# Kernel optimization log

Hardware: AMD Instinct MI355X
Metric: run time of the kernel (lower is better)

## Reference

```python
import jax, jax.numpy as jnp
import numpy as np

CHEB_K = 3
EMBED_DIM = 16
N_NODES = 2048
DIM = 64


def setup_inputs() -> dict:
    key = jax.random.key(0)
    k1, k2, k3, k4 = jax.random.split(key, 4)
    B, N, T, D = 16, N_NODES, 12, DIM
    x = jax.random.normal(k1, (B, N, T, D), dtype=jnp.float32)
    node_embeddings = jax.random.normal(k2, (N, EMBED_DIM), dtype=jnp.float32)
    # xavier-uniform-ish init for pools
    wp_bound = float(np.sqrt(6.0 / (EMBED_DIM * CHEB_K * D + D)))
    weights_pool = jax.random.uniform(k3, (EMBED_DIM, CHEB_K, D, D), dtype=jnp.float32,
                                      minval=-wp_bound, maxval=wp_bound)
    bias_pool = jax.random.uniform(k4, (EMBED_DIM, D), dtype=jnp.float32)
    return {"x": x, "node_embeddings": node_embeddings,
            "weights_pool": weights_pool, "bias_pool": bias_pool}


def reference(x, node_embeddings, weights_pool, bias_pool):
    B, N, T, D = x.shape
    cheb_k = weights_pool.shape[1]
    # [B,N,T,D] -> [B*T, N, D]
    xr = jnp.transpose(x, (0, 2, 1, 3)).reshape(B * T, N, D)
    # adaptive adjacency: row-softmax of relu gram matrix  [N,N]
    supports = jax.nn.softmax(jax.nn.relu(node_embeddings @ node_embeddings.T), axis=1)
    # Chebyshev polynomial basis of the adaptive support
    support_set = [jnp.eye(N, dtype=supports.dtype), supports]
    for _ in range(2, cheb_k):
        support_set.append(2.0 * supports @ support_set[-1] - support_set[-2])
    supports_k = jnp.stack(support_set, axis=0)  # [K,N,N]
    # hypernetwork: per-node weights/bias from embeddings
    weights = jnp.einsum('nd,dkio->nkio', node_embeddings, weights_pool)  # [N,K,D,D]
    bias = node_embeddings @ bias_pool  # [N,D]
    # graph conv: gather K-hop aggregates, then per-node grouped GEMM
    x_g = jnp.einsum('knm,bmc->bnkc', supports_k, xr)  # [B*T,N,K,D]
    x_gconv = jnp.einsum('bnki,nkio->bno', x_g, weights) + bias  # [B*T,N,D]
    return jnp.transpose(x_gconv.reshape(B, T, N, D), (0, 2, 1, 3))
```

## Files before the change

### kernel.cpp

```cpp
#include <hip/hip_runtime.h>
#include <hip/hip_bf16.h>

#define N_NODES 2048
#define EMB 16
#define NT 12
#define BT 192
#define C_COLS 12288
#define TD 768
#define BSTRIDE (N_NODES * TD)
#define KDIM 2048

typedef unsigned short u16;
typedef unsigned int u32;
typedef __attribute__((ext_vector_type(8))) __bf16 bf16x8;
typedef __attribute__((ext_vector_type(8))) u16 u16x8;
typedef __attribute__((ext_vector_type(4))) float f32x4;

__device__ __forceinline__ u16 f2bfu(float f) {
    u32 u = __float_as_uint(f);
    return (u16)((u + 0x7FFFu + ((u >> 16) & 1u)) >> 16);
}
__device__ __forceinline__ float bfu2f(u16 h) {
    return __uint_as_float(((u32)h) << 16);
}

__device__ __forceinline__ void gl2lds16(const void* g, void* l) {
    __builtin_amdgcn_global_load_lds(
        (const __attribute__((address_space(1))) u32*)g,
        (__attribute__((address_space(3))) u32*)l, 16, 0, 0);
}

__device__ __forceinline__ int cswz(int col, int row) {
    return (col & ~63) | ((((col >> 3) ^ row) & 7) << 3) | (col & 7);
}

__global__ void supports_kernel(const float* __restrict__ E, u16* __restrict__ Sb)
{
    __shared__ float en[EMB];
    __shared__ float red[256];
    const int n = blockIdx.x;
    const int tid = threadIdx.x;
    if (tid < EMB) en[tid] = E[n * EMB + tid];
    __syncthreads();

    float v[8];
    float mx = 0.0f;
    #pragma unroll
    for (int j = 0; j < 8; ++j) {
        const int m = tid + j * 256;
        const float* em = E + m * EMB;
        float acc = 0.f;
        #pragma unroll
        for (int d = 0; d < EMB; ++d) acc += en[d] * em[d];
        acc = fmaxf(acc, 0.f);
        v[j] = acc;
        mx = fmaxf(mx, acc);
    }
    red[tid] = mx;
    __syncthreads();
    for (int s = 128; s > 0; s >>= 1) {
        if (tid < s) red[tid] = fmaxf(red[tid], red[tid + s]);
        __syncthreads();
    }
    mx = red[0];
    __syncthreads();

    float sum = 0.f;
    #pragma unroll
    for (int j = 0; j < 8; ++j) { v[j] = __expf(v[j] - mx); sum += v[j]; }
    red[tid] = sum;
    __syncthreads();
    for (int s = 128; s > 0; s >>= 1) {
        if (tid < s) red[tid] += red[tid + s];
        __syncthreads();
    }
    const float inv = 1.f / red[0];
    #pragma unroll
    for (int j = 0; j < 8; ++j)
        Sb[(size_t)n * KDIM + tid + j * 256] = f2bfu(v[j] * inv);
}

__global__ void supports2_kernel(const float* __restrict__ E, u16* __restrict__ Sb)
{
    __shared__ float en[EMB];
    __shared__ float red[256];
    const int n = blockIdx.x;
    const int tid = threadIdx.x;
    if (tid < EMB) en[tid] = E[n * EMB + tid];
    __syncthreads();

    float v[8];
    float mx = 0.0f;
    #pragma unroll
    for (int j = 0; j < 8; ++j) {
        const int m = tid + j * 256;
        const float* em = E + m * EMB;
        float acc = 0.f;
        #pragma unroll
        for (int d = 0; d < EMB; ++d) acc += en[d] * em[d];
        acc = fmaxf(acc, 0.f);
        v[j] = acc;
        mx = fmaxf(mx, acc);
    }
    red[tid] = mx;
    __syncthreads();
    for (int s = 128; s > 0; s >>= 1) {
        if (tid < s) red[tid] = fmaxf(red[tid], red[tid + s]);
        __syncthreads();
    }
    mx = red[0];
    __syncthreads();

    float sum = 0.f;
    #pragma unroll
    for (int j = 0; j < 8; ++j) { v[j] = __expf(v[j] - mx); sum += v[j]; }
    red[tid] = sum;
    __syncthreads();
    for (int s = 128; s > 0; s >>= 1) {
        if (tid < s) red[tid] += red[tid + s];
        __syncthreads();
    }
    const float inv = 1.f / red[0];
    #pragma unroll
    for (int j = 0; j < 8; ++j) {
        const int m = tid + j * 256;
        Sb[(size_t)n * KDIM + cswz(m, n)] = f2bfu(v[j] * inv);
    }
}

__global__ void strans_kernel(const u16* __restrict__ Sb, u16* __restrict__ SbT)
{
    __shared__ u16 T[64][65];
    const int tid = threadIdx.x;
    const int n0 = blockIdx.y * 64;
    const int j0 = blockIdx.x * 64;
    const int lc = tid & 63;
    const int rg = tid >> 6;
    #pragma unroll
    for (int j = 0; j < 16; ++j) {
        const int r = j * 4 + rg;
        const u16 vv = Sb[(size_t)(n0 + r) * KDIM + j0 + lc];
        const int jt = ((((lc >> 3) ^ (n0 + r)) & 7) << 3) | (lc & 7);
        T[jt][r] = vv;
    }
    __syncthreads();
    #pragma unroll
    for (int j = 0; j < 16; ++j) {
        const int jj = j * 4 + rg;
        const int cs = ((((lc >> 3) ^ (j0 + jj)) & 7) << 3) | (lc & 7);
        SbT[(size_t)(j0 + jj) * KDIM + n0 + cs] = T[jj][lc];
    }
}

__global__ void xcast_kernel(const float* __restrict__ x, u16* __restrict__ XbT, int c0g)
{
    __shared__ u16 tile[64][65];
    const int tid = threadIdx.x;
    const int cg = c0g + blockIdx.x * 64;
    const int b = cg / TD;
    const int r0 = cg - b * TD;
    const int m0 = blockIdx.y * 64;
    const float* xp = x + (size_t)b * BSTRIDE + (size_t)m0 * TD + r0;

    const int lc = tid & 63;
    const int rg = tid >> 6;
    #pragma unroll
    for (int j = 0; j < 16; ++j) {
        const int mr = j * 4 + rg;
        tile[lc][mr] = f2bfu(xp[(size_t)mr * TD + lc]);
    }
    __syncthreads();
    u16* op = XbT + (size_t)(blockIdx.x * 64) * KDIM + m0;
    #pragma unroll
    for (int j = 0; j < 16; ++j) {
        const int cr = j * 4 + rg;
        op[(size_t)cr * KDIM + lc] = tile[cr][lc];
    }
}

__global__ void xcast2_kernel(const float* __restrict__ x, u16* __restrict__ XbT)
{
    __shared__ u16 tile[64][65];
    const int tid = threadIdx.x;
    const int cg = blockIdx.x * 64;
    const int b = cg / TD;
    const int r0 = cg - b * TD;
    const int m0 = blockIdx.y * 64;
    const float* xp = x + (size_t)b * BSTRIDE + (size_t)m0 * TD + r0;

    const int lc = tid & 63;
    const int rg = tid >> 6;
    #pragma unroll
    for (int j = 0; j < 16; ++j) {
        const int mr = j * 4 + rg;
        tile[lc][mr] = f2bfu(xp[(size_t)mr * TD + lc]);
    }
    __syncthreads();
    u16* op = XbT + (size_t)cg * KDIM + m0;
    #pragma unroll
    for (int j = 0; j < 16; ++j) {
        const int cr = j * 4 + rg;
        const int ls = ((((lc >> 3) ^ cr) & 7) << 3) | (lc & 7);
        op[(size_t)cr * KDIM + ls] = tile[cr][lc];
    }
}

template <int MODE>
__launch_bounds__(512, 2)
__global__ void gemm256(const u16* __restrict__ A, const u16* __restrict__ B,
                        u16* __restrict__ O1, u16* __restrict__ O2)
{
    __shared__ char smem[131072];
    const int tid = threadIdx.x;
    const int lane = tid & 63;
    const int w = tid >> 6;
    const int wm = w >> 2, wn = w & 3;
    const int ln15 = lane & 15, quad = lane >> 4;

    const int m0 = blockIdx.y * 256;
    const int c0 = blockIdx.x * 256;

    const int srow = lane >> 3;
    const int sbyte = (lane & 7) * 16;
    const char* gA = (const char*)A + (size_t)(m0 + w * 32 + srow) * 4096 + sbyte;
    const char* gB = (const char*)B + (size_t)(c0 + w * 32 + srow) * 4096 + sbyte;
    char* lA = smem + w * 4096;
    char* lB = smem + 32768 + w * 4096;

    auto stage = [&](int t, int buf) {
        #pragma unroll
        for (int j = 0; j < 4; ++j) {
            gl2lds16(gA + (size_t)j * 32768 + (size_t)t * 128,
                     lA + buf * 65536 + j * 1024);
            gl2lds16(gB + (size_t)j * 32768 + (size_t)t * 128,
                     lB + buf * 65536 + j * 1024);
        }
    };

    f32x4 acc[8][4] = {};
    const int arow0 = wm * 128 + ln15;
    const int brow0 = wn * 64 + ln15;
    const int xorm = (ln15 & 7) << 4;

    auto phase = [&](const char* Ab, const char* Bb, int kh) {
        const int koff = (kh * 64 + quad * 16) ^ xorm;
        bf16x8 af[8], bg[4];
        #pragma unroll
        for (int mi = 0; mi < 8; ++mi)
            af[mi] = *(const bf16x8*)(Ab + (arow0 + mi * 16) * 128 + koff);
        #pragma unroll
        for (int ni = 0; ni < 4; ++ni)
            bg[ni] = *(const bf16x8*)(Bb + (brow0 + ni * 16) * 128 + koff);
        asm volatile("s_waitcnt lgkmcnt(0)" ::: "memory");
        __builtin_amdgcn_sched_barrier(0);
        __builtin_amdgcn_s_setprio(1);
        #pragma unroll
        for (int mi = 0; mi < 8; ++mi)
            #pragma unroll
            for (int ni = 0; ni < 4; ++ni)
                acc[mi][ni] = __builtin_amdgcn_mfma_f32_16x16x32_bf16(
                    af[mi], bg[ni], acc[mi][ni], 0, 0, 0);
        __builtin_amdgcn_s_setprio(0);
        __builtin_amdgcn_sched_barrier(0);
        __builtin_amdgcn_s_barrier();
    };

    const char* b0A = smem;
    const char* b0B = smem + 32768;
    const char* b1A = smem + 65536;
    const char* b1B = smem + 98304;

    const int NTI = KDIM / 64;
    stage(0, 0);
    stage(1, 1);

    #pragma unroll 1
    for (int it = 0; it < NTI / 2; ++it) {
        const int t0 = 2 * it;
        if (it > 0) stage(t0 + 1, 1);
        asm volatile("s_waitcnt vmcnt(8)" ::: "memory");
        __builtin_amdgcn_sched_barrier(0);
        __builtin_amdgcn_s_barrier();

        phase(b0A, b0B, 0);
        phase(b0A, b0B, 1);

        if (t0 + 2 < NTI) {
            stage(t0 + 2, 0);
            asm volatile("s_waitcnt vmcnt(8)" ::: "memory");
        } else {
            asm volatile("s_waitcnt vmcnt(0)" ::: "memory");
        }
        __builtin_amdgcn_sched_barrier(0);
        __builtin_amdgcn_s_barrier();

        phase(b1A, b1B, 0);
        phase(b1A, b1B, 1);
    }

    const int mbase = m0 + wm * 128 + quad * 4;
    const int cbase = c0 + wn * 64 + ln15;
    if (MODE == 0) {
        #pragma unroll
        for (int mi = 0; mi < 8; ++mi) {
            #pragma unroll
            for (int ni = 0; ni < 4; ++ni) {
                const f32x4 v = acc[mi][ni];
                const int cc = cbase + ni * 16;
                #pragma unroll
                for (int r = 0; r < 4; ++r) {
                    const int mm = mbase + mi * 16 + r;
                    const float t2 = 2.f * v[r] - ((mm == cc) ? 1.f : 0.f);
                    O1[(size_t)mm * KDIM + cswz(cc, mm)] = f2bfu(t2);
                }
            }
        }
    } else {
        u16* Ob = (m0 < 2048) ? O1 : O2;
        const int mb = (m0 < 2048) ? mbase : (mbase - 2048);
        #pragma unroll
        for (int mi = 0; mi < 8; ++mi) {
            #pragma unroll
            for (int ni = 0; ni < 4; ++ni) {
                const f32x4 v = acc[mi][ni];
                const int cc = cbase + ni * 16;
                u16* orow = Ob + (size_t)(mb + mi * 16) * C_COLS + cc;
                orow[0 * C_COLS] = f2bfu(v.x);
                orow[1 * C_COLS] = f2bfu(v.y);
                orow[2 * C_COLS] = f2bfu(v.z);
                orow[3 * C_COLS] = f2bfu(v.w);
            }
        }
    }
}

__launch_bounds__(256, 2)
__global__ void gemm128s(const u16* __restrict__ A, const u16* __restrict__ B,
                         u16* __restrict__ O1)
{
    __shared__ char smem[65536];
    const int tid = threadIdx.x;
    const int lane = tid & 63;
    const int w = tid >> 6;
    const int wm = w >> 1, wn = w & 1;
    const int ln15 = lane & 15, quad = lane >> 4;

    const int m0 = blockIdx.y * 128;
    const int c0 = blockIdx.x * 128;

    const int srow = lane >> 3;
    const int sbyte = (lane & 7) * 16;
    const char* gA = (const char*)A + (size_t)(m0 + w * 32 + srow) * 4096 + sbyte;
    const char* gB = (const char*)B + (size_t)(c0 + w * 32 + srow) * 4096 + sbyte;
    char* lA = smem + w * 4096;
    char* lB = smem + 16384 + w * 4096;

    auto stage = [&](int t, int buf) {
        #pragma unroll
        for (int j = 0; j < 4; ++j) {
            gl2lds16(gA + (size_t)j * 32768 + (size_t)t * 128,
                     lA + buf * 32768 + j * 1024);
            gl2lds16(gB + (size_t)j * 32768 + (size_t)t * 128,
                     lB + buf * 32768 + j * 1024);
        }
    };

    f32x4 acc[4][4] = {};
    const int arow0 = wm * 64 + ln15;
    const int brow0 = wn * 64 + ln15;
    const int xorm = (ln15 & 7) << 4;

    auto phase = [&](const char* Ab, const char* Bb, int kh) {
        const int koff = (kh * 64 + quad * 16) ^ xorm;
        bf16x8 af[4], bg[4];
        #pragma unroll
        for (int mi = 0; mi < 4; ++mi)
            af[mi] = *(const bf16x8*)(Ab + (arow0 + mi * 16) * 128 + koff);
        #pragma unroll
        for (int ni = 0; ni < 4; ++ni)
            bg[ni] = *(const bf16x8*)(Bb + (brow0 + ni * 16) * 128 + koff);
        asm volatile("s_waitcnt lgkmcnt(0)" ::: "memory");
        __builtin_amdgcn_sched_barrier(0);
        __builtin_amdgcn_s_setprio(1);
        #pragma unroll
        for (int mi = 0; mi < 4; ++mi)
            #pragma unroll
            for (int ni = 0; ni < 4; ++ni)
                acc[mi][ni] = __builtin_amdgcn_mfma_f32_16x16x32_bf16(
                    af[mi], bg[ni], acc[mi][ni], 0, 0, 0);
        __builtin_amdgcn_s_setprio(0);
        __builtin_amdgcn_sched_barrier(0);
        __builtin_amdgcn_s_barrier();
    };

    const int NTI = KDIM / 64;
    stage(0, 0);
    stage(1, 1);

    #pragma unroll 1
    for (int it = 0; it < NTI / 2; ++it) {
        const int t0 = 2 * it;
        if (it > 0) stage(t0 + 1, 1);
        asm volatile("s_waitcnt vmcnt(8)" ::: "memory");
        __builtin_amdgcn_sched_barrier(0);
        __builtin_amdgcn_s_barrier();

        phase(smem, smem + 16384, 0);
        phase(smem, smem + 16384, 1);

        if (t0 + 2 < NTI) {
            stage(t0 + 2, 0);
            asm volatile("s_waitcnt vmcnt(8)" ::: "memory");
        } else {
            asm volatile("s_waitcnt vmcnt(0)" ::: "memory");
        }
        __builtin_amdgcn_sched_barrier(0);
        __builtin_amdgcn_s_barrier();

        phase(smem + 32768, smem + 49152, 0);
        phase(smem + 32768, smem + 49152, 1);
    }

    const int mbase = m0 + wm * 64 + quad * 4;
    const int cbase = c0 + wn * 64 + ln15;
    #pragma unroll
    for (int mi = 0; mi < 4; ++mi) {
        #pragma unroll
        for (int ni = 0; ni < 4; ++ni) {
            const f32x4 v = acc[mi][ni];
            const int cc = cbase + ni * 16;
            #pragma unroll
            for (int r = 0; r < 4; ++r) {
                const int mm = mbase + mi * 16 + r;
                const float t2 = 2.f * v[r] - ((mm == cc) ? 1.f : 0.f);
                O1[(size_t)mm * KDIM + cswz(cc, mm)] = f2bfu(t2);
            }
        }
    }
}

template <int MODE>
__launch_bounds__(256, 3)
__global__ void mfma_gemm(const u16* __restrict__ A,
                          const u16* __restrict__ B,
                          u16* __restrict__ OutT,
                          u16* __restrict__ OutRow,
                          const u16* __restrict__ Xc,
                          int c0g)
{
    __shared__ char smem[16384];
    char* As = smem;
    char* Bs = smem + 8192;

    const int tid = threadIdx.x;
    const int lane = tid & 63;
    const int w = tid >> 6;
    const int wm = w >> 1, wn = w & 1;
    const int ln15 = lane & 15, quad = lane >> 4;

    const int m0 = blockIdx.y * 128;
    const int cb = blockIdx.x * 128;

    const int q0 = 2 * w, q1 = 2 * w + 1;
    const int srow = lane >> 2;
    const int skol = (lane & 3) * 8;
    const u16* ga0 = A + (size_t)(m0 + q0 * 16 + srow) * KDIM + skol;
    const u16* ga1 = A + (size_t)(m0 + q1 * 16 + srow) * KDIM + skol;
    const u16* gb0 = B + (size_t)(cb + q0 * 16 + srow) * KDIM + skol;
    const u16* gb1 = B + (size_t)(cb + q1 * 16 + srow) * KDIM + skol;
    char* la0 = As + q0 * 1024;
    char* la1 = As + q1 * 1024;
    char* lb0 = Bs + q0 * 1024;
    char* lb1 = Bs + q1 * 1024;

    f32x4 acc[4][4] = {};

    for (int k0 = 0; k0 < KDIM; k0 += 32) {
        __syncthreads();
        gl2lds16(ga0, la0);
        gl2lds16(ga1, la1);
        gl2lds16(gb0, lb0);
        gl2lds16(gb1, lb1);
        ga0 += 32; ga1 += 32; gb0 += 32; gb1 += 32;
        __syncthreads();

        bf16x8 af[4], bg[4];
        #pragma unroll
        for (int i = 0; i < 4; ++i) {
            af[i] = *(const bf16x8*)(As + ((wm * 64 + i * 16 + ln15) * 64 + quad * 16));
            bg[i] = *(const bf16x8*)(Bs + ((wn * 64 + i * 16 + ln15) * 64 + quad * 16));
        }
        #pragma unroll
        for (int mi = 0; mi < 4; ++mi)
            #pragma unroll
            for (int ni = 0; ni < 4; ++ni)
                acc[mi][ni] = __builtin_amdgcn_mfma_f32_16x16x32_bf16(
                    af[mi], bg[ni], acc[mi][ni], 0, 0, 0);
    }

    const int mbase = m0 + wm * 64 + quad * 4;
    const int cbase = cb + wn * 64 + ln15;
    #pragma unroll
    for (int mi = 0; mi < 4; ++mi) {
        #pragma unroll
        for (int ni = 0; ni < 4; ++ni) {
            const f32x4 v = acc[mi][ni];
            const int mm = mbase + mi * 16;
            const int cc = cbase + ni * 16;
            if (MODE == 0) {
                ushort4 u;
                u.x = f2bfu(v.x); u.y = f2bfu(v.y); u.z = f2bfu(v.z); u.w = f2bfu(v.w);
                *(ushort4*)(OutT + (size_t)cc * KDIM + mm) = u;
                u16* orow = OutRow + (size_t)mm * C_COLS + c0g + cc;
                orow[0 * C_COLS] = u.x;
                orow[1 * C_COLS] = u.y;
                orow[2 * C_COLS] = u.z;
                orow[3 * C_COLS] = u.w;
            } else {
                const ushort4 xv = *(const ushort4*)(Xc + (size_t)cc * KDIM + mm);
                u16* orow = OutRow + (size_t)mm * C_COLS + c0g + cc;
                orow[0 * C_COLS] = f2bfu(2.f * v.x - bfu2f(xv.x));
                orow[1 * C_COLS] = f2bfu(2.f * v.y - bfu2f(xv.y));
                orow[2 * C_COLS] = f2bfu(2.f * v.z - bfu2f(xv.z));
                orow[3 * C_COLS] = f2bfu(2.f * v.w - bfu2f(xv.w));
            }
        }
    }
}

__launch_bounds__(256, 2)
__global__ void whyper_kernel(const float* __restrict__ E,
                              const float* __restrict__ Wp,
                              u16* __restrict__ Wrow)
{
    __shared__ float Es[32][16];
    const int tid = threadIdx.x;
    const int kt = blockIdx.x;
    const int n0 = blockIdx.y * 32;
    for (int i = tid; i < 512; i += 256)
        Es[i >> 4][i & 15] = E[(n0 + (i >> 4)) * EMB + (i & 15)];
    __syncthreads();

    const int o = tid & 63;
    const int kq = tid >> 6;
    #pragma unroll 1
    for (int it = 0; it < 6; ++it) {
        const int ki = kt * 24 + it * 4 + kq;
        const float* wp = Wp + (size_t)ki * 64 + o;
        float wv[EMB];
        #pragma unroll
        for (int d = 0; d < EMB; ++d) wv[d] = wp[(size_t)d * 12288];
        #pragma unroll 4
        for (int nn = 0; nn < 32; ++nn) {
            float a = 0.f;
            #pragma unroll
            for (int d = 0; d < EMB; ++d) a = fmaf(Es[nn][d], wv[d], a);
            Wrow[(size_t)(n0 + nn) * 12288 + (size_t)ki * 64 + o] = f2bfu(a);
        }
    }
}

__launch_bounds__(256, 4)
__global__ void gconv_mfma2_kernel(const float* __restrict__ x,
                                   const float* __restrict__ E,
                                   const float* __restrict__ Bp,
                                   const u16* __restrict__ Wrow,
                                   const u16* __restrict__ Y1,
                                   const u16* __restrict__ Y2,
                                   float* __restrict__ Out)
{
    __shared__ char WsB[24576];
    __shared__ float en[EMB];
    __shared__ float bias[64];

    const int n = blockIdx.x;
    const int tid = threadIdx.x;
    const int lane = tid & 63;
    const int w = tid >> 6;

    if (tid < EMB) en[tid] = E[n * EMB + tid];

    {
        const u16* Wn = Wrow + (size_t)n * 12288;
        ushort4 va[6][2];
        #pragma unroll
        for (int j = 0; j < 6; ++j) {
            const int c = tid + j * 256;
            va[j][0] = *(const ushort4*)(Wn + c * 8);
            va[j][1] = *(const ushort4*)(Wn + c * 8 + 4);
        }
        #pragma unroll
        for (int j = 0; j < 6; ++j) {
            const int c = tid + j * 256;
            const int ki = c >> 3;
            const int o0 = (c & 7) * 8;
            const int kb = ((ki >> 3) << 4) | ((ki & 7) * 2);
            const u16 vals[8] = { va[j][0].x, va[j][0].y, va[j][0].z, va[j][0].w,
                                  va[j][1].x, va[j][1].y, va[j][1].z, va[j][1].w };
            #pragma unroll
            for (int e = 0; e < 8; ++e) {
                const int o = o0 + e;
                *(u16*)(WsB + o * 384 + (kb ^ ((o & 7) << 4))) = vals[e];
            }
        }
    }
    __syncthreads();

    if (tid < 64) {
        float a = 0.f;
        #pragma unroll
        for (int d = 0; d < EMB; ++d) a = fmaf(en[d], Bp[d * 64 + tid], a);
        bias[tid] = a;
    }
    __syncthreads();

    const int ln15 = lane & 15, quad = lane >> 4;
    const int q16 = quad * 16;
    const int m0w = w * 48;

    int rowb[4], msk[4];
    #pragma unroll
    for (int ni = 0; ni < 4; ++ni) {
        const int o = ni * 16 + ln15;
        rowb[ni] = o * 384;
        msk[ni] = (o & 7) << 4;
    }

    const float* xb[3];
    size_t yo[3];
    #pragma unroll
    for (int mi = 0; mi < 3; ++mi) {
        const int bt = m0w + mi * 16 + ln15;
        const int b = bt / NT, t = bt - b * NT;
        xb[mi] = x + (size_t)b * BSTRIDE + (size_t)n * TD + (size_t)t * 64 + quad * 8;
        yo[mi] = (size_t)n * C_COLS + (size_t)bt * 64 + quad * 8;
    }

    f32x4 acc[3][4] = {};

    #pragma unroll
    for (int ks = 0; ks < 2; ++ks) {
        bf16x8 af[3];
        #pragma unroll
        for (int mi = 0; mi < 3; ++mi) {
            const float* p = xb[mi] + ks * 32;
            const f32x4 lo = *(const f32x4*)p;
            const f32x4 hi = *(const f32x4*)(p + 4);
            u16x8 u;
            u[0] = f2bfu(lo.x); u[1] = f2bfu(lo.y); u[2] = f2bfu(lo.z); u[3] = f2bfu(lo.w);
            u[4] = f2bfu(hi.x); u[5] = f2bfu(hi.y); u[6] = f2bfu(hi.z); u[7] = f2bfu(hi.w);
            af[mi] = *(const bf16x8*)&u;
        }
        bf16x8 bg[4];
        #pragma unroll
        for (int ni = 0; ni < 4; ++ni)
            bg[ni] = *(const bf16x8*)(WsB + rowb[ni] + ((ks * 64 + q16) ^ msk[ni]));
        #pragma unroll
        for (int mi = 0; mi < 3; ++mi)
            #pragma unroll
            for (int ni = 0; ni < 4; ++ni)
                acc[mi][ni] = __builtin_amdgcn_mfma_f32_16x16x32_bf16(
                    af[mi], bg[ni], acc[mi][ni], 0, 0, 0);
    }

    const u16* ybase[2] = { Y1, Y2 };
    #pragma unroll
    for (int s = 0; s < 2; ++s) {
        const u16* Yb = ybase[s];
        #pragma unroll
        for (int ks = 0; ks < 2; ++ks) {
            bf16x8 af[3];
            #pragma unroll
            for (int mi = 0; mi < 3; ++mi)
                af[mi] = *(const bf16x8*)(Yb + yo[mi] + ks * 32);
            bf16x8 bg[4];
            #pragma unroll
            for (int ni = 0; ni < 4; ++ni)
                bg[ni] = *(const bf16x8*)(WsB + rowb[ni] + 128 + s * 128
                                          + ((ks * 64 + q16) ^ msk[ni]));
            #pragma unroll
            for (int mi = 0; mi < 3; ++mi)
                #pragma unroll
                for (int ni = 0; ni < 4; ++ni)
                    acc[mi][ni] = __builtin_amdgcn_mfma_f32_16x16x32_bf16(
                        af[mi], bg[ni], acc[mi][ni], 0, 0, 0);
        }
    }

    float bv[4];
    #pragma unroll
    for (int ni = 0; ni < 4; ++ni) bv[ni] = bias[ni * 16 + ln15];

    #pragma unroll
    for (int mi = 0; mi < 3; ++mi) {
        const int rowb2 = m0w + mi * 16 + quad * 4;
        #pragma unroll
        for (int r = 0; r < 4; ++r) {
            const int bt = rowb2 + r;
            const int b = bt / NT, t = bt - b * NT;
            float* op = Out + (((size_t)(b * N_NODES + n)) * NT + t) * 64 + ln15;
            #pragma unroll
            for (int ni = 0; ni < 4; ++ni)
                op[ni * 16] = acc[mi][ni][r] + bv[ni];
        }
    }
}

__launch_bounds__(256, 4)
__global__ void gconv_mfma_kernel(const float* __restrict__ x,
                                  const float* __restrict__ E,
                                  const float* __restrict__ Wp,
                                  const float* __restrict__ Bp,
                                  const u16* __restrict__ Y1,
                                  const u16* __restrict__ Y2,
                                  float* __restrict__ Out)
{
    __shared__ u16 Ws[64][200];
    __shared__ float en[EMB];
    __shared__ float bias[64];

    const int n = blockIdx.x;
    const int tid = threadIdx.x;
    if (tid < EMB) en[tid] = E[n * EMB + tid];
    __syncthreads();

    {
        const int o = tid & 63;
        const int kio = tid >> 6;
        #pragma unroll 4
        for (int j = 0; j < 48; ++j) {
            const int ki = j * 4 + kio;
            const float* wp = Wp + ki * 64 + o;
            float a = 0.f;
            #pragma unroll
            for (int d = 0; d < EMB; ++d) a = fmaf(en[d], wp[d * 12288], a);
            Ws[o][ki] = f2bfu(a);
        }
        if (tid < 64) {
            float a = 0.f;
            #pragma unroll
            for (int d = 0; d < EMB; ++d) a = fmaf(en[d], Bp[d * 64 + tid], a);
            bias[tid] = a;
        }
    }
    __syncthreads();

    const int lane = tid & 63;
    const int w = tid >> 6;
    const int ln15 = lane & 15, quad = lane >> 4;
    const int m0w = w * 48;

    const float* xb[3];
    size_t yo[3];
    #pragma unroll
    for (int mi = 0; mi < 3; ++mi) {
        const int bt = m0w + mi * 16 + ln15;
        const int b = bt / NT, t = bt - b * NT;
        xb[mi] = x + (size_t)b * BSTRIDE + (size_t)n * TD + (size_t)t * 64 + quad * 8;
        yo[mi] = (size_t)n * C_COLS + (size_t)bt * 64 + quad * 8;
    }

    f32x4 acc[3][4] = {};

    #pragma unroll
    for (int ks = 0; ks < 2; ++ks) {
        bf16x8 af[3];
        #pragma unroll
        for (int mi = 0; mi < 3; ++mi) {
            const float* p = xb[mi] + ks * 32;
            const f32x4 lo = *(const f32x4*)p;
            const f32x4 hi = *(const f32x4*)(p + 4);
            u16x8 u;
            u[0] = f2bfu(lo.x); u[1] = f2bfu(lo.y); u[2] = f2bfu(lo.z); u[3] = f2bfu(lo.w);
            u[4] = f2bfu(hi.x); u[5] = f2bfu(hi.y); u[6] = f2bfu(hi.z); u[7] = f2bfu(hi.w);
            af[mi] = *(const bf16x8*)&u;
        }
        bf16x8 bg[4];
        #pragma unroll
        for (int ni = 0; ni < 4; ++ni)
            bg[ni] = *(const bf16x8*)&Ws[ni * 16 + ln15][ks * 32 + quad * 8];
        #pragma unroll
        for (int mi = 0; mi < 3; ++mi)
            #pragma unroll
            for (int ni = 0; ni < 4; ++ni)
                acc[mi][ni] = __builtin_amdgcn_mfma_f32_16x16x32_bf16(
                    af[mi], bg[ni], acc[mi][ni], 0, 0, 0);
    }

    const u16* ybase[2] = { Y1, Y2 };
    #pragma unroll
    for (int s = 0; s < 2; ++s) {
        const u16* Yb = ybase[s];
        #pragma unroll
        for (int ks = 0; ks < 2; ++ks) {
            bf16x8 af[3];
            #pragma unroll
            for (int mi = 0; mi < 3; ++mi)
                af[mi] = *(const bf16x8*)(Yb + yo[mi] + ks * 32);
            bf16x8 bg[4];
            #pragma unroll
            for (int ni = 0; ni < 4; ++ni)
                bg[ni] = *(const bf16x8*)&Ws[ni * 16 + ln15][64 + s * 64 + ks * 32 + quad * 8];
            #pragma unroll
            for (int mi = 0; mi < 3; ++mi)
                #pragma unroll
                for (int ni = 0; ni < 4; ++ni)
                    acc[mi][ni] = __builtin_amdgcn_mfma_f32_16x16x32_bf16(
                        af[mi], bg[ni], acc[mi][ni], 0, 0, 0);
        }
    }

    float bv[4];
    #pragma unroll
    for (int ni = 0; ni < 4; ++ni) bv[ni] = bias[ni * 16 + ln15];

    #pragma unroll
    for (int mi = 0; mi < 3; ++mi) {
        const int rowb = m0w + mi * 16 + quad * 4;
        #pragma unroll
        for (int r = 0; r < 4; ++r) {
            const int bt = rowb + r;
            const int b = bt / NT, t = bt - b * NT;
            float* op = Out + (((size_t)(b * N_NODES + n)) * NT + t) * 64 + ln15;
            #pragma unroll
            for (int ni = 0; ni < 4; ++ni)
                op[ni * 16] = acc[mi][ni][r] + bv[ni];
        }
    }
}

extern "C" void kernel_launch(void* const* d_in, const int* in_sizes, int n_in,
                              void* d_out, int out_size, void* d_ws, size_t ws_size,
                              hipStream_t stream)
{
    const float* x  = (const float*)d_in[0];
    const float* E  = (const float*)d_in[1];
    const float* Wp = (const float*)d_in[2];
    const float* Bp = (const float*)d_in[3];
    float* Out = (float*)d_out;

    const size_t MiB = 1024 * 1024;

    if (ws_size >= 216 * MiB) {
        u16* Sb    = (u16*)d_ws;
        u16* T2b   = (u16*)((char*)d_ws + 8 * MiB);
        u16* SbT   = (u16*)((char*)d_ws + 16 * MiB);
        u16* Y1row = (u16*)((char*)d_ws + 24 * MiB);
        u16* Y2row = (u16*)((char*)d_ws + 72 * MiB);
        u16* XbT   = (u16*)((char*)d_ws + 120 * MiB);
        u16* Wbuf  = (u16*)((char*)d_ws + 168 * MiB);

        supports2_kernel<<<N_NODES, 256, 0, stream>>>(E, Sb);
        strans_kernel<<<dim3(32, 32), 256, 0, stream>>>(Sb, SbT);
        gemm128s<<<dim3(16, 16), 256, 0, stream>>>(Sb, SbT, T2b);
        xcast2_kernel<<<dim3(192, 32), 256, 0, stream>>>(x, XbT);
        gemm256<1><<<dim3(48, 16), 512, 0, stream>>>(Sb, XbT, Y1row, Y2row);

        whyper_kernel<<<dim3(8, 64), 256, 0, stream>>>(E, Wp, Wbuf);
        gconv_mfma2_kernel<<<N_NODES, 256, 0, stream>>>(x, E, Bp, Wbuf, Y1row, Y2row, Out);
        return;
    }

    u16* Sb    = (u16*)d_ws;
    u16* Y1row = (u16*)((char*)d_ws + 8 * MiB);
    u16* Y2row = (u16*)((char*)d_ws + 56 * MiB);
    char* chunkbase = (char*)d_ws + 104 * MiB;

    size_t wall_off = 0;
    bool newpath = false;
    if (ws_size >= 160 * MiB) {
        wall_off = ((ws_size - 48 * MiB) / 256) * 256;
        if (wall_off >= 112 * MiB) newpath = true;
    }
    const size_t budget = newpath ? wall_off : ws_size;

    const int cands[5] = {1, 2, 3, 6, 12};
    int nc = 12;
    for (int i = 0; i < 5; ++i) {
        const size_t chunk_bytes = (size_t)(C_COLS / cands[i]) * KDIM * 2;
        if (104 * MiB + 2 * chunk_bytes <= budget) { nc = cands[i]; break; }
    }
    const int CW = C_COLS / nc;
    u16* XbTc = (u16*)chunkbase;
    u16* Y1Tc = (u16*)(chunkbase + (size_t)CW * KDIM * 2);
    u16* Wbuf = (u16*)((char*)d_ws + wall_off);

    supports_kernel<<<N_NODES, 256, 0, stream>>>(E, Sb);

    if (newpath) {
        whyper_kernel<<<dim3(8, 64), 256, 0, stream>>>(E, Wp, Wbuf);
    }

    for (int c = 0; c < nc; ++c) {
        const int c0g = c * CW;
        xcast_kernel<<<dim3(CW / 64, 32), 256, 0, stream>>>(x, XbTc, c0g);
        mfma_gemm<0><<<dim3(CW / 128, 16), 256, 0, stream>>>(Sb, XbTc, Y1Tc, Y1row, nullptr, c0g);
        mfma_gemm<1><<<dim3(CW / 128, 16), 256, 0, stream>>>(Sb, Y1Tc, nullptr, Y2row, XbTc, c0g);
    }

    if (newpath)
        gconv_mfma2_kernel<<<N_NODES, 256, 0, stream>>>(x, E, Bp, Wbuf, Y1row, Y2row, Out);
    else
        gconv_mfma_kernel<<<N_NODES, 256, 0, stream>>>(x, E, Wp, Bp, Y1row, Y2row, Out);
}
```

Measured before the change: 492.0 us.

## Restructure GEMM main loop into four sub-phases with interleaved staging

Rewrites the gemm256 K-loop: the shared-memory layout is split into two 64-byte-wide k-halves with a new XOR swizzle. Each tile's compute is broken into four half-M sub-phases, and global-to-LDS loads for A and B halves are issued between them. The aim is finer overlap of memory loads with MFMA work and lower register pressure, since B fragments are reused and only four A fragments are live at a time. In exchange it adds more barriers per iteration and a more delicate vmcnt accounting that must stay correct across buffer reuse.

```diff
diff --git a/kernel.cpp b/kernel.cpp
--- a/kernel.cpp
+++ b/kernel.cpp
@@ -220,82 +220,154 @@
     const int m0 = blockIdx.y * 256;
     const int c0 = blockIdx.x * 256;
 
-    const int srow = lane >> 3;
-    const int sbyte = (lane & 7) * 16;
-    const char* gA = (const char*)A + (size_t)(m0 + w * 32 + srow) * 4096 + sbyte;
-    const char* gB = (const char*)B + (size_t)(c0 + w * 32 + srow) * 4096 + sbyte;
-    char* lA = smem + w * 4096;
-    char* lB = smem + 32768 + w * 4096;
-
-    auto stage = [&](int t, int buf) {
-        #pragma unroll
-        for (int j = 0; j < 4; ++j) {
-            gl2lds16(gA + (size_t)j * 32768 + (size_t)t * 128,
-                     lA + buf * 65536 + j * 1024);
-            gl2lds16(gB + (size_t)j * 32768 + (size_t)t * 128,
-                     lB + buf * 65536 + j * 1024);
-        }
+    const int xq = lane & 3;
+    u32 offA[2][2], offB[2][2];
+    #pragma unroll
+    for (int kh = 0; kh < 2; ++kh)
+        #pragma unroll
+        for (int j = 0; j < 2; ++j) {
+            const int rl = w * 32 + j * 16 + (lane >> 2);
+            const int P = (rl >> 1) & 3;
+            const int ct = kh * 4 + (xq ^ P);
+            const int slot = (ct ^ (rl & 7)) & 7;
+            offA[kh][j] = (u32)((m0 + rl) * 4096 + slot * 16);
+            offB[kh][j] = (u32)((c0 + rl) * 4096 + slot * 16);
+        }
+    char* ldA[2][2];
+    char* ldB[2][2];
+    #pragma unroll
+    for (int kh = 0; kh < 2; ++kh)
+        #pragma unroll
+        for (int j = 0; j < 2; ++j) {
+            ldA[kh][j] = smem + kh * 16384 + (w * 32 + j * 16) * 64;
+            ldB[kh][j] = smem + 32768 + kh * 16384 + (w * 32 + j * 16) * 64;
+        }
+
+    auto stageA = [&](int t, int buf, int kh) {
+        #pragma unroll
+        for (int j = 0; j < 2; ++j)
+            gl2lds16((const char*)A + (size_t)offA[kh][j] + (size_t)t * 128,
+                     ldA[kh][j] + buf * 65536);
     };
+    auto stageB = [&](int t, int buf, int kh) {
+        #pragma unroll
+        for (int j = 0; j < 2; ++j)
+            gl2lds16((const char*)B + (size_t)offB[kh][j] + (size_t)t * 128,
+                     ldB[kh][j] + buf * 65536);
+    };
 
     f32x4 acc[8][4] = {};
+    bf16x8 bg[4];
     const int arow0 = wm * 128 + ln15;
     const int brow0 = wn * 64 + ln15;
-    const int xorm = (ln15 & 7) << 4;
-
-    auto phase = [&](const char* Ab, const char* Bb, int kh) {
-        const int koff = (kh * 64 + quad * 16) ^ xorm;
-        bf16x8 af[8], bg[4];
-        #pragma unroll
-        for (int mi = 0; mi < 8; ++mi)
-            af[mi] = *(const bf16x8*)(Ab + (arow0 + mi * 16) * 128 + koff);
-        #pragma unroll
-        for (int ni = 0; ni < 4; ++ni)
-            bg[ni] = *(const bf16x8*)(Bb + (brow0 + ni * 16) * 128 + koff);
-        asm volatile("s_waitcnt lgkmcnt(0)" ::: "memory");
-        __builtin_amdgcn_sched_barrier(0);
-        __builtin_amdgcn_s_setprio(1);
-        #pragma unroll
-        for (int mi = 0; mi < 8; ++mi)
+    const int koff = ((quad ^ ((ln15 >> 1) & 3)) & 3) * 16;
+
+    const int NTI = KDIM / 64;
+
+    stageA(0, 0, 0); stageB(0, 0, 0); stageA(0, 0, 1); stageB(0, 0, 1);
+    stageB(1, 1, 0); stageA(1, 1, 0); stageB(1, 1, 1);
+    asm volatile("s_waitcnt vmcnt(6)" ::: "memory");
+    __builtin_amdgcn_sched_barrier(0);
+    __builtin_amdgcn_s_barrier();
+
+    #pragma unroll 1
+    for (int t = 0; t < NTI; ++t) {
+        const int cur = t & 1;
+        const char* Ab = smem + cur * 65536;
+        const char* Bb = Ab + 32768;
+
+        {
+            bf16x8 af[4];
             #pragma unroll
             for (int ni = 0; ni < 4; ++ni)
-                acc[mi][ni] = __builtin_amdgcn_mfma_f32_16x16x32_bf16(
-                    af[mi], bg[ni], acc[mi][ni], 0, 0, 0);
-        __builtin_amdgcn_s_setprio(0);
-        __builtin_amdgcn_sched_barrier(0);
-        __builtin_amdgcn_s_barrier();
-    };
-
-    const char* b0A = smem;
-    const char* b0B = smem + 32768;
-    const char* b1A = smem + 65536;
-    const char* b1B = smem + 98304;
-
-    const int NTI = KDIM / 64;
-    stage(0, 0);
-    stage(1, 1);
-
-    #pragma unroll 1
-    for (int it = 0; it < NTI / 2; ++it) {
-        const int t0 = 2 * it;
-        if (it > 0) stage(t0 + 1, 1);
-        asm volatile("s_waitcnt vmcnt(8)" ::: "memory");
-        __builtin_amdgcn_sched_barrier(0);
-        __builtin_amdgcn_s_barrier();
-
-        phase(b0A, b0B, 0);
-        phase(b0A, b0B, 1);
-
-        if (t0 + 2 < NTI) {
-            stage(t0 + 2, 0);
-            asm volatile("s_waitcnt vmcnt(8)" ::: "memory");
-        } else {
-            asm volatile("s_waitcnt vmcnt(0)" ::: "memory");
-        }
-        __builtin_amdgcn_sched_barrier(0);
-        __builtin_amdgcn_s_barrier();
-
-        phase(b1A, b1B, 0);
-        phase(b1A, b1B, 1);
+                bg[ni] = *(const bf16x8*)(Bb + (brow0 + ni * 16) * 64 + koff);
+            #pragma unroll
+            for (int mi = 0; mi < 4; ++mi)
+                af[mi] = *(const bf16x8*)(Ab + (arow0 + mi * 16) * 64 + koff);
+            if (t + 1 < NTI) stageA(t + 1, cur ^ 1, 1);
+            __builtin_amdgcn_s_barrier();
+            asm volatile("s_waitcnt lgkmcnt(0)" ::: "memory");
+            __builtin_amdgcn_sched_barrier(0);
+            __builtin_amdgcn_s_setprio(1);
+            #pragma unroll
+            for (int mi = 0; mi < 4; ++mi)
+                #pragma unroll
+                for (int ni = 0; ni < 4; ++ni)
+                    acc[mi][ni] = __builtin_amdgcn_mfma_f32_16x16x32_bf16(
+                        af[mi], bg[ni], acc[mi][ni], 0, 0, 0);
+            __builtin_amdgcn_s_setprio(0);
+            __builtin_amdgcn_sched_barrier(0);
+            __builtin_amdgcn_s_barrier();
+        }
+        {
+            bf16x8 af[4];
+            #pragma unroll
+            for (int mi = 0; mi < 4; ++mi)
+                af[mi] = *(const bf16x8*)(Ab + (arow0 + (4 + mi) * 16) * 64 + koff);
+            if (t + 2 < NTI) stageB(t + 2, cur, 0);
+            __builtin_amdgcn_s_barrier();
+            asm volatile("s_waitcnt lgkmcnt(0)" ::: "memory");
+            __builtin_amdgcn_sched_barrier(0);
+            __builtin_amdgcn_s_setprio(1);
+            #pragma unroll
+            for (int mi = 0; mi < 4; ++mi)
+                #pragma unroll
+                for (int ni = 0; ni < 4; ++ni)
+                    acc[4 + mi][ni] = __builtin_amdgcn_mfma_f32_16x16x32_bf16(
+                        af[mi], bg[ni], acc[4 + mi][ni], 0, 0, 0);
+            __builtin_amdgcn_s_setprio(0);
+            __builtin_amdgcn_sched_barrier(0);
+            __builtin_amdgcn_s_barrier();
+        }
+        {
+            bf16x8 af[4];
+            #pragma unroll
+            for (int ni = 0; ni < 4; ++ni)
+                bg[ni] = *(const bf16x8*)(Bb + 16384 + (brow0 + ni * 16) * 64 + koff);
+            #pragma unroll
+            for (int mi = 0; mi < 4; ++mi)
+                af[mi] = *(const bf16x8*)(Ab + 16384 + (arow0 + mi * 16) * 64 + koff);
+            if (t + 2 < NTI) stageA(t + 2, cur, 0);
+            __builtin_amdgcn_s_barrier();
+            asm volatile("s_waitcnt lgkmcnt(0)" ::: "memory");
+            __builtin_amdgcn_sched_barrier(0);
+            __builtin_amdgcn_s_setprio(1);
+            #pragma unroll
+            for (int mi = 0; mi < 4; ++mi)
+                #pragma unroll
+                for (int ni = 0; ni < 4; ++ni)
+                    acc[mi][ni] = __builtin_amdgcn_mfma_f32_16x16x32_bf16(
+                        af[mi], bg[ni], acc[mi][ni], 0, 0, 0);
+            __builtin_amdgcn_s_setprio(0);
+            __builtin_amdgcn_sched_barrier(0);
+            __builtin_amdgcn_s_barrier();
+        }
+        {
+            bf16x8 af[4];
+            #pragma unroll
+            for (int mi = 0; mi < 4; ++mi)
+                af[mi] = *(const bf16x8*)(Ab + 16384 + (arow0 + (4 + mi) * 16) * 64 + koff);
+            if (t + 2 < NTI) {
+                stageB(t + 2, cur, 1);
+                asm volatile("s_waitcnt vmcnt(6)" ::: "memory");
+            } else {
+                asm volatile("s_waitcnt vmcnt(0)" ::: "memory");
+            }
+            __builtin_amdgcn_sched_barrier(0);
+            __builtin_amdgcn_s_barrier();
+            asm volatile("s_waitcnt lgkmcnt(0)" ::: "memory");
+            __builtin_amdgcn_sched_barrier(0);
+            __builtin_amdgcn_s_setprio(1);
+            #pragma unroll
+            for (int mi = 0; mi < 4; ++mi)
+                #pragma unroll
+                for (int ni = 0; ni < 4; ++ni)
+                    acc[4 + mi][ni] = __builtin_amdgcn_mfma_f32_16x16x32_bf16(
+                        af[mi], bg[ni], acc[4 + mi][ni], 0, 0, 0);
+            __builtin_amdgcn_s_setprio(0);
+            __builtin_amdgcn_sched_barrier(0);
+            __builtin_amdgcn_s_barrier();
+        }
     }
 
     const int mbase = m0 + wm * 128 + quad * 4;
```

Result: no change. 498.9 us (+1.4%).
